# Performance work log

Hardware: AMD Instinct MI355X
Metric: run time of the kernel (lower is better)

## Reference

```python
import jax, jax.numpy as jnp
import numpy as np


def setup_inputs() -> dict:
    key = jax.random.key(0)
    ks = jax.random.split(key, 8)
    B, T, D, E = 16, 1024, 1024, 64
    s = lambda fan: 1.0 / np.sqrt(fan)
    return {
        "seq": jax.random.normal(ks[0], (B, T, D), jnp.float32),
        "pi": jax.random.uniform(ks[1], (E,), jnp.float32),
        "beta_raw": jnp.full((D,), 2.1972246, jnp.float32),  # logit(0.9)
        "p1_w": jax.random.normal(ks[2], (4 * D, 2 * D), jnp.float32) * s(2 * D),
        "p1_b": jnp.zeros((4 * D,), jnp.float32),
        "p2_w": jax.random.normal(ks[3], (D, 4 * D), jnp.float32) * s(4 * D),
        "p2_b": jnp.zeros((D,), jnp.float32),
        "W_w": jax.random.normal(ks[4], (E, D), jnp.float32) * s(D),
        "W_b": jnp.zeros((E,), jnp.float32),
    }


def reference(seq, pi, beta_raw, p1_w, p1_b, p2_w, p2_b, W_w, W_b):
    B, T, D = seq.shape
    beta = jax.nn.sigmoid(beta_raw)  # (D,), per-channel EMA coefficient
    x = jnp.transpose(seq[:, : T - 1, :], (1, 0, 2))  # (T-1, B, D), steps 0..T-2

    # Sequential EMA recurrence h_t = beta*h_{t-1} + x_t (h_{-1}=0)
    def step(h, x_t):
        h = beta * h + x_t
        return h, h

    _, hs = jax.lax.scan(step, jnp.zeros((B, D), seq.dtype), x)  # (T-1, B, D)

    # Predictor MLP over all timesteps at once (use_beta + use_ant branch)
    inp = jnp.concatenate([x, hs], axis=-1)  # (T-1, B, 2D)
    hid = jax.nn.relu(jnp.einsum('tbi,hi->tbh', inp, p1_w) + p1_b)  # (T-1, B, 4D)
    x_hat = jnp.einsum('tbh,dh->tbd', hid, p2_w) + p2_b  # (T-1, B, D)

    # Linear router + pi scaling
    logits = (jnp.einsum('tbd,ed->tbe', x_hat, W_w) + W_b) * pi  # (T-1, B, E)
    return logits, x_hat
```

## Files before the change

kernel.cpp:

```cpp
#include <hip/hip_runtime.h>
#include <hip/hip_bf16.h>
#include <cstdint>
#include <cstddef>

using bf16 = __hip_bfloat16;
typedef __bf16 bf16x8 __attribute__((ext_vector_type(8)));
typedef float f32x4 __attribute__((ext_vector_type(4)));

#define BB 16
#define TT 1024
#define DD 1024
#define EE 64
#define MREAL 16368
#define MPAD  16384
#define NCHUNK 16
#define CHUNK 64

__device__ __forceinline__ void gload_lds16(const void* g, void* l) {
  __builtin_amdgcn_global_load_lds((const __attribute__((address_space(1))) void*)g,
                                   (__attribute__((address_space(3))) void*)l,
                                   16, 0, 0);
}

__device__ __forceinline__ float sigmoidf_(float x) {
  return 1.0f / (1.0f + __expf(-x));
}

__global__ void f2b(const float* __restrict__ src, bf16* __restrict__ dst, int n) {
  int i = (blockIdx.x * blockDim.x + threadIdx.x) * 8;
  if (i < n) {
    float4 v0 = *reinterpret_cast<const float4*>(src + i);
    float4 v1 = *reinterpret_cast<const float4*>(src + i + 4);
    alignas(16) bf16 tmp[8];
    tmp[0] = __float2bfloat16(v0.x); tmp[1] = __float2bfloat16(v0.y);
    tmp[2] = __float2bfloat16(v0.z); tmp[3] = __float2bfloat16(v0.w);
    tmp[4] = __float2bfloat16(v1.x); tmp[5] = __float2bfloat16(v1.y);
    tmp[6] = __float2bfloat16(v1.z); tmp[7] = __float2bfloat16(v1.w);
    *reinterpret_cast<float4*>(dst + i) = *reinterpret_cast<const float4*>(tmp);
  }
}

__global__ void ema_ends(const float* __restrict__ seq, const float* __restrict__ beta_raw,
                         float* __restrict__ ends) {
  int tid = blockIdx.x * blockDim.x + threadIdx.x;
  int d = tid & (DD - 1);
  int b = (tid >> 10) & (BB - 1);
  int c = tid >> 14;
  float beta = sigmoidf_(beta_raw[d]);
  int t0 = c * CHUNK;
  int len = min(CHUNK, (TT - 1) - t0);
  const float* p = seq + (size_t)b * TT * DD + (size_t)t0 * DD + d;
  float h = 0.0f;
#pragma unroll 8
  for (int j = 0; j < len; ++j) h = fmaf(beta, h, p[(size_t)j * DD]);
  ends[tid] = h;
}

__global__ void ema_carry(const float* __restrict__ ends, const float* __restrict__ beta_raw,
                          float* __restrict__ carry) {
  int tid = blockIdx.x * blockDim.x + threadIdx.x;
  int d = tid & (DD - 1);
  float beta = sigmoidf_(beta_raw[d]);
  float bl = beta;
  bl *= bl; bl *= bl; bl *= bl; bl *= bl; bl *= bl; bl *= bl;
  float run = 0.0f;
#pragma unroll
  for (int c = 0; c < NCHUNK; ++c) {
    carry[c * (BB * DD) + tid] = run;
    run = ends[c * (BB * DD) + tid] + bl * run;
  }
}

__global__ void ema_write(const float* __restrict__ seq, const float* __restrict__ beta_raw,
                          const float* __restrict__ carry, bf16* __restrict__ A) {
  int tid = blockIdx.x * blockDim.x + threadIdx.x;
  int d = tid & (DD - 1);
  int b = (tid >> 10) & (BB - 1);
  int c = tid >> 14;
  float beta = sigmoidf_(beta_raw[d]);
  int t0 = c * CHUNK;
  int len = min(CHUNK, (TT - 1) - t0);
  const float* p = seq + (size_t)b * TT * DD + (size_t)t0 * DD + d;
  float h = carry[tid];
#pragma unroll 4
  for (int j = 0; j < len; ++j) {
    float x = p[(size_t)j * DD];
    h = fmaf(beta, h, x);
    size_t m = (size_t)(t0 + j) * BB + b;
    A[m * (2 * DD) + d]      = __float2bfloat16(x);
    A[m * (2 * DD) + DD + d] = __float2bfloat16(h);
  }
}


#define RD_A(d, fb)                                                          \
  _Pragma("unroll")                                                          \
  for (int f = 0; f < 4; ++f)                                                \
    _Pragma("unroll")                                                        \
    for (int s = 0; s < 2; ++s)                                              \
      a[f][s] = *reinterpret_cast<const bf16x8*>(                            \
          &lds[(d) * 32768 + ArdB + ((fb) + f) * 1024 + roff[s]]);

#define RD_B(d, j0)                                                          \
  _Pragma("unroll")                                                          \
  for (int jj = 0; jj < 2; ++jj)                                             \
    _Pragma("unroll")                                                        \
    for (int s = 0; s < 2; ++s)                                              \
      b[(j0) + jj][s] = *reinterpret_cast<const bf16x8*>(                    \
          &lds[(d) * 32768 + BrdB + ((j0) + jj) * 1024 + roff[s]]);

#define STAGE_A(d, h, kq)                                                    \
  {                                                                          \
    _Pragma("unroll")                                                        \
    for (int t = 0; t < 2; ++t)                                              \
      gload_lds16(gA + ((size_t)((h) * 128 + t * 8) * K + (kq) * 64),        \
                  &lds[(d) * 32768 + (h) * 8192 + stbase + t * 512]);        \
  }

#define STAGE_B(d, h, kq)                                                    \
  {                                                                          \
    _Pragma("unroll")                                                        \
    for (int t = 0; t < 2; ++t)                                              \
      gload_lds16(gB + ((size_t)((h) * 128 + t * 8) * K + (kq) * 64),        \
                  &lds[(d) * 32768 + 16384 + (h) * 8192 + stbase + t * 512]); \
  }

#define MFMA_Q(fb, j0)                                                       \
  _Pragma("unroll")                                                          \
  for (int s = 0; s < 2; ++s)                                                \
    _Pragma("unroll")                                                        \
    for (int f = 0; f < 4; ++f)                                              \
      _Pragma("unroll")                                                      \
      for (int j = 0; j < 2; ++j)                                            \
        acc[(fb) + f][(j0) + j] = __builtin_amdgcn_mfma_f32_16x16x32_bf16(   \
            a[f][s], b[(j0) + j][s], acc[(fb) + f][(j0) + j], 0, 0, 0);

#define PH_MID()                                                             \
  __builtin_amdgcn_s_barrier();                                              \
  asm volatile("s_waitcnt lgkmcnt(0)" ::: "memory");                         \
  __builtin_amdgcn_sched_barrier(0);                                         \
  __builtin_amdgcn_s_setprio(1);

#define PH_END()                                                             \
  __builtin_amdgcn_s_setprio(0);                                             \
  __builtin_amdgcn_sched_barrier(0);                                         \
  __builtin_amdgcn_s_barrier();

#define KTILE(d)                                                             \
  {                                                                          \
    const int kA = (q + 1 < NT) ? (q + 1) : (NT - 1);                        \
    const int kB = (q + 2 < NT) ? (q + 2) : (NT - 1);                        \
                                                   \
    RD_A(d, 0);                                                              \
    RD_B(d, 0);                                                              \
    STAGE_A((d) ^ 1, 0, kA);                                                 \
    asm volatile("s_waitcnt lgkmcnt(8)" ::: "memory");                       \
    PH_MID(); MFMA_Q(0, 0); PH_END();                                        \
                                                   \
    RD_B(d, 2);                                                              \
    STAGE_A((d) ^ 1, 1, kA);                                                 \
    PH_MID(); MFMA_Q(0, 2); PH_END();                                        \
                                                   \
    RD_A(d, 4);                                                              \
    STAGE_B((d), 0, kB);                                                     \
    PH_MID(); MFMA_Q(4, 2); PH_END();                                        \
                                                   \
    STAGE_B((d), 1, kB);                                                     \
    asm volatile("s_waitcnt vmcnt(4)" ::: "memory");                         \
    PH_MID(); MFMA_Q(4, 0); PH_END();                                        \
    ++q;                                                                     \
  }

template <bool RELU, bool DUAL_OUT>
__global__ __launch_bounds__(512, 2)
void gemm8(const bf16* __restrict__ A, const bf16* __restrict__ B,
           const float* __restrict__ bias, bf16* __restrict__ outb,
           float* __restrict__ outf, int N, int K) {
  __shared__ bf16 lds[65536];
  const int tid  = threadIdx.x;
  const int wave = tid >> 6;
  const int lane = tid & 63;
  const int wm = wave >> 2;
  const int wn = wave & 3;

  const int gx   = gridDim.x;
  const int nwg  = gx * gridDim.y;
  const int orig = blockIdx.y * gx + blockIdx.x;
  const int swz  = (orig & 7) * (nwg >> 3) + (orig >> 3);
  const int bm = (swz / gx) * 256;
  const int bn = (swz % gx) * 256;

  const int srow = lane >> 3;
  const int scg  = (lane & 7) ^ srow;
  const bf16* gA = A + (size_t)(bm + wave * 16 + srow) * K + scg * 8;
  const bf16* gB = B + (size_t)(bn + wave * 16 + srow) * K + scg * 8;
  const int stbase = wave * 1024;

  int roff[2];
#pragma unroll
  for (int s = 0; s < 2; ++s)
    roff[s] = (lane & 15) * 64 + (((s * 4 + (lane >> 4)) ^ (lane & 7)) * 8);
  const int ArdB = wm * 8192;
  const int BrdB = 16384 + (wn >> 1) * 8192 + (wn & 1) * 4096;

  f32x4 acc[8][4] = {};
  bf16x8 a[4][2], b[4][2];
  const int NT = K >> 6;
  int q = 0;

  STAGE_A(0, 0, 0);
  STAGE_A(0, 1, 0);
  STAGE_B(0, 0, 0);
  STAGE_B(0, 1, 0);
  STAGE_B(1, 0, 1);
  STAGE_B(1, 1, 1);
  asm volatile("s_waitcnt vmcnt(4)" ::: "memory");
  __builtin_amdgcn_s_barrier();

#pragma unroll 1
  for (int it = 0; it < (NT >> 1); ++it) {
    KTILE(0);
    KTILE(1);
  }
  asm volatile("s_waitcnt vmcnt(0)" ::: "memory");

  float bv[4];
  int   ncol[4];
#pragma unroll
  for (int j = 0; j < 4; ++j) {
    ncol[j] = bn + wn * 64 + j * 16 + (lane & 15);
    bv[j]   = bias[ncol[j]];
  }
#pragma unroll
  for (int f = 0; f < 8; ++f) {
    const int m0 = bm + wm * 128 + f * 16 + (lane >> 4) * 4;
#pragma unroll
    for (int j = 0; j < 4; ++j) {
      const int n = ncol[j];
#pragma unroll
      for (int r = 0; r < 4; ++r) {
        float v = acc[f][j][r] + bv[j];
        if (RELU) v = fmaxf(v, 0.0f);
        const int m = m0 + r;
        outb[(size_t)m * N + n] = __float2bfloat16(v);
        if (DUAL_OUT) {
          if (m < MREAL) outf[(size_t)m * N + n] = v;
        }
      }
    }
  }
}

__global__ __launch_bounds__(256)
void gemm_router(const bf16* __restrict__ A, const bf16* __restrict__ B,
                 const float* __restrict__ Wb, const float* __restrict__ pi,
                 float* __restrict__ out) {
  const int K = DD;
  __shared__ alignas(16) bf16 As[64 * 32];
  __shared__ alignas(16) bf16 Bs[64 * 32];
  const int tid  = threadIdx.x;
  const int wave = tid >> 6;
  const int lane = tid & 63;
  const int bm = blockIdx.x * 64;
  const int srow = wave * 16 + (lane >> 2);
  const int scol = (lane & 3) * 8;
  const bf16* gA = A + (size_t)(bm + srow) * K + scol;
  const bf16* gB = B + (size_t)srow * K + scol;
  bf16* lA = &As[srow * 32 + scol];
  bf16* lB = &Bs[srow * 32 + scol];
  const int lr = lane & 15;
  const int quad = lane >> 4;
  f32x4 acc[4] = {};
  for (int k0 = 0; k0 < K; k0 += 32) {
    __syncthreads();
    gload_lds16(gA + k0, lA);
    gload_lds16(gB + k0, lB);
    __syncthreads();
    bf16x8 af = *reinterpret_cast<const bf16x8*>(&As[(wave * 16 + lr) * 32 + quad * 8]);
#pragma unroll
    for (int j = 0; j < 4; ++j) {
      bf16x8 bf_ = *reinterpret_cast<const bf16x8*>(&Bs[(j * 16 + lr) * 32 + quad * 8]);
      acc[j] = __builtin_amdgcn_mfma_f32_16x16x32_bf16(af, bf_, acc[j], 0, 0, 0);
    }
  }
#pragma unroll
  for (int j = 0; j < 4; ++j) {
    const int e = j * 16 + lr;
    const float wb = Wb[e], pv = pi[e];
#pragma unroll
    for (int r = 0; r < 4; ++r) {
      const int m = bm + wave * 16 + quad * 4 + r;
      if (m < MREAL) out[(size_t)m * EE + e] = (acc[j][r] + wb) * pv;
    }
  }
}

extern "C" void kernel_launch(void* const* d_in, const int* in_sizes, int n_in,
                              void* d_out, int out_size, void* d_ws, size_t ws_size,
                              hipStream_t stream) {
  const float* seq      = (const float*)d_in[0];
  const float* pi       = (const float*)d_in[1];
  const float* beta_raw = (const float*)d_in[2];
  const float* p1_w     = (const float*)d_in[3];
  const float* p1_b     = (const float*)d_in[4];
  const float* p2_w     = (const float*)d_in[5];
  const float* p2_b     = (const float*)d_in[6];
  const float* W_w      = (const float*)d_in[7];
  const float* W_b      = (const float*)d_in[8];

  constexpr size_t A_off    = 0;
  constexpr size_t A_sz     = (size_t)MPAD * 2 * DD * sizeof(bf16);
  constexpr size_t W1_off   = A_off + A_sz;
  constexpr size_t W1_sz    = (size_t)4 * DD * 2 * DD * sizeof(bf16);
  constexpr size_t HID_off  = W1_off + W1_sz;
  constexpr size_t HID_sz   = (size_t)MPAD * 4 * DD * sizeof(bf16);
  constexpr size_t W2_off   = HID_off + HID_sz;
  constexpr size_t W2_sz    = (size_t)DD * 4 * DD * sizeof(bf16);
  constexpr size_t W3_off   = W2_off + W2_sz;
  constexpr size_t W3_sz    = (size_t)EE * DD * sizeof(bf16);
  constexpr size_t ENDS_off = W3_off + W3_sz;
  constexpr size_t ENDS_sz  = (size_t)NCHUNK * BB * DD * sizeof(float);
  constexpr size_t CARRY_off = ENDS_off + ENDS_sz;

  char* ws = (char*)d_ws;
  bf16*  Abuf = (bf16*)(ws + A_off);
  bf16*  W1   = (bf16*)(ws + W1_off);
  bf16*  HID  = (bf16*)(ws + HID_off);
  bf16*  W2   = (bf16*)(ws + W2_off);
  bf16*  W3   = (bf16*)(ws + W3_off);
  float* ENDS = (float*)(ws + ENDS_off);
  float* CARRY = (float*)(ws + CARRY_off);
  bf16*  XH   = (bf16*)(ws + A_off);

  float* out_logits = (float*)d_out;
  float* out_xhat   = out_logits + (size_t)MREAL * EE;

  f2b<<<(4 * DD * 2 * DD / 8 + 255) / 256, 256, 0, stream>>>(p1_w, W1, 4 * DD * 2 * DD);
  f2b<<<(DD * 4 * DD / 8 + 255) / 256, 256, 0, stream>>>(p2_w, W2, DD * 4 * DD);
  f2b<<<(EE * DD / 8 + 255) / 256, 256, 0, stream>>>(W_w, W3, EE * DD);

  ema_ends<<<NCHUNK * BB * DD / 256, 256, 0, stream>>>(seq, beta_raw, ENDS);
  ema_carry<<<BB * DD / 256, 256, 0, stream>>>(ENDS, beta_raw, CARRY);
  ema_write<<<NCHUNK * BB * DD / 256, 256, 0, stream>>>(seq, beta_raw, CARRY, Abuf);
  (void)hipMemsetAsync(ws + A_off + (size_t)MREAL * 2 * DD * sizeof(bf16), 0,
                       (size_t)(MPAD - MREAL) * 2 * DD * sizeof(bf16), stream);

  gemm8<true, false><<<dim3(4 * DD / 256, MPAD / 256), 512, 0, stream>>>(
      Abuf, W1, p1_b, HID, nullptr, 4 * DD, 2 * DD);

  gemm8<false, true><<<dim3(DD / 256, MPAD / 256), 512, 0, stream>>>(
      HID, W2, p2_b, XH, out_xhat, DD, 4 * DD);

  gemm_router<<<MPAD / 64, 256, 0, stream>>>(XH, W3, W_b, pi, out_logits);
}
```

Measured before the change: 574.3 us.

## Switch GEMM inner loop to 32x32x16 MFMA with reorganized LDS reads

Replaces the 16x16x32 bf16 MFMA tiling in the main GEMM with 32x32x16 MFMA instructions, each wave holding 4x2 32x32 accumulator tiles. The LDS read pattern, swizzle offsets, phase schedule and epilogue row mapping are rewritten to match the new fragment layout. It also drops the explicit lgkmcnt waits and sched_barriers between phases and leaves wait placement to the compiler. The larger MFMA shape is meant to raise operand reuse per instruction and cut LDS reads and instruction count. The trade-offs are a changed register footprint and possible hazards from the relaxed waits.

```diff
diff --git a/kernel.cpp b/kernel.cpp
--- a/kernel.cpp
+++ b/kernel.cpp
@@ -6,6 +6,7 @@
 using bf16 = __hip_bfloat16;
 typedef __bf16 bf16x8 __attribute__((ext_vector_type(8)));
 typedef float f32x4 __attribute__((ext_vector_type(4)));
+typedef float f32x16 __attribute__((ext_vector_type(16)));
 
 #define BB 16
 #define TT 1024
@@ -93,21 +94,19 @@
 }
 
 
-#define RD_A(d, fb)                                                          \
+#define RD_A2(d, m0)                                                         \
   _Pragma("unroll")                                                          \
-  for (int f = 0; f < 4; ++f)                                                \
+  for (int mf = 0; mf < 2; ++mf)                                             \
     _Pragma("unroll")                                                        \
-    for (int s = 0; s < 2; ++s)                                              \
-      a[f][s] = *reinterpret_cast<const bf16x8*>(                            \
-          &lds[(d) * 32768 + ArdB + ((fb) + f) * 1024 + roff[s]]);
-
-#define RD_B(d, j0)                                                          \
+    for (int ks = 0; ks < 4; ++ks)                                           \
+      a[mf][ks] = *reinterpret_cast<const bf16x8*>(                          \
+          &lds[(d) * 32768 + aB0 + ((m0) + mf) * 2048 + pgs[ks]]);
+
+#define RD_B4(d, nf, breg)                                                   \
   _Pragma("unroll")                                                          \
-  for (int jj = 0; jj < 2; ++jj)                                             \
-    _Pragma("unroll")                                                        \
-    for (int s = 0; s < 2; ++s)                                              \
-      b[(j0) + jj][s] = *reinterpret_cast<const bf16x8*>(                    \
-          &lds[(d) * 32768 + BrdB + ((j0) + jj) * 1024 + roff[s]]);
+  for (int ks = 0; ks < 4; ++ks)                                             \
+    breg[ks] = *reinterpret_cast<const bf16x8*>(                             \
+        &lds[(d) * 32768 + bO[nf] + pgs[ks]]);
 
 #define STAGE_A(d, h, kq)                                                    \
   {                                                                          \
@@ -125,49 +124,42 @@
                   &lds[(d) * 32768 + 16384 + (h) * 8192 + stbase + t * 512]); \
   }
 
-#define MFMA_Q(fb, j0)                                                       \
+#define PH_MFMA(m0, breg, nf)                                                \
+  __builtin_amdgcn_s_barrier();                                              \
+  __builtin_amdgcn_s_setprio(1);                                             \
   _Pragma("unroll")                                                          \
-  for (int s = 0; s < 2; ++s)                                                \
-    _Pragma("unroll")                                                        \
-    for (int f = 0; f < 4; ++f)                                              \
-      _Pragma("unroll")                                                      \
-      for (int j = 0; j < 2; ++j)                                            \
-        acc[(fb) + f][(j0) + j] = __builtin_amdgcn_mfma_f32_16x16x32_bf16(   \
-            a[f][s], b[(j0) + j][s], acc[(fb) + f][(j0) + j], 0, 0, 0);
-
-#define PH_MID()                                                             \
-  __builtin_amdgcn_s_barrier();                                              \
-  asm volatile("s_waitcnt lgkmcnt(0)" ::: "memory");                         \
-  __builtin_amdgcn_sched_barrier(0);                                         \
-  __builtin_amdgcn_s_setprio(1);
-
-#define PH_END()                                                             \
+  for (int ks = 0; ks < 4; ++ks) {                                           \
+    acc[(m0)][nf] = __builtin_amdgcn_mfma_f32_32x32x16_bf16(                 \
+        a[0][ks], breg[ks], acc[(m0)][nf], 0, 0, 0);                         \
+    acc[(m0) + 1][nf] = __builtin_amdgcn_mfma_f32_32x32x16_bf16(             \
+        a[1][ks], breg[ks], acc[(m0) + 1][nf], 0, 0, 0);                     \
+  }                                                                          \
   __builtin_amdgcn_s_setprio(0);                                             \
-  __builtin_amdgcn_sched_barrier(0);                                         \
   __builtin_amdgcn_s_barrier();
 
 #define KTILE(d)                                                             \
   {                                                                          \
     const int kA = (q + 1 < NT) ? (q + 1) : (NT - 1);                        \
     const int kB = (q + 2 < NT) ? (q + 2) : (NT - 1);                        \
-                                                   \
-    RD_A(d, 0);                                                              \
-    RD_B(d, 0);                                                              \
+                                                       \
+    RD_A2(d, 0);                                                             \
+    RD_B4(d, 0, b0);                                                         \
     STAGE_A((d) ^ 1, 0, kA);                                                 \
-    asm volatile("s_waitcnt lgkmcnt(8)" ::: "memory");                       \
-    PH_MID(); MFMA_Q(0, 0); PH_END();                                        \
-                                                   \
-    RD_B(d, 2);                                                              \
+    PH_MFMA(0, b0, 0);                                                       \
+                                                       \
+    RD_B4(d, 1, b1);                                                         \
     STAGE_A((d) ^ 1, 1, kA);                                                 \
-    PH_MID(); MFMA_Q(0, 2); PH_END();                                        \
-                                                   \
-    RD_A(d, 4);                                                              \
+    PH_MFMA(0, b1, 1);                                                       \
+                                                       \
+    RD_A2(d, 2);                                                             \
+    asm volatile("" ::: "memory");   \
     STAGE_B((d), 0, kB);                                                     \
-    PH_MID(); MFMA_Q(4, 2); PH_END();                                        \
-                                                   \
+    PH_MFMA(2, b1, 1);                                                       \
+                                                       \
+    asm volatile("" ::: "memory");                                           \
     STAGE_B((d), 1, kB);                                                     \
     asm volatile("s_waitcnt vmcnt(4)" ::: "memory");                         \
-    PH_MID(); MFMA_Q(4, 0); PH_END();                                        \
+    PH_MFMA(2, b0, 0);                                                       \
     ++q;                                                                     \
   }
 
@@ -196,15 +188,20 @@
   const bf16* gB = B + (size_t)(bn + wave * 16 + srow) * K + scg * 8;
   const int stbase = wave * 1024;
 
-  int roff[2];
-#pragma unroll
-  for (int s = 0; s < 2; ++s)
-    roff[s] = (lane & 15) * 64 + (((s * 4 + (lane >> 4)) ^ (lane & 7)) * 8);
-  const int ArdB = wm * 8192;
-  const int BrdB = 16384 + (wn >> 1) * 8192 + (wn & 1) * 4096;
-
-  f32x4 acc[8][4] = {};
-  bf16x8 a[4][2], b[4][2];
+  int pgs[4];
+#pragma unroll
+  for (int ks = 0; ks < 4; ++ks)
+    pgs[ks] = (((ks * 2 + (lane >> 5)) ^ (lane & 7)) * 8);
+  const int aB0 = wm * 8192 + (lane & 31) * 64;
+  int bO[2];
+#pragma unroll
+  for (int nf = 0; nf < 2; ++nf) {
+    const int rb = wn * 64 + nf * 32 + (lane & 31);
+    bO[nf] = 16384 + (rb >> 7) * 8192 + (rb & 127) * 64;
+  }
+
+  f32x16 acc[4][2] = {};
+  bf16x8 a[2][4], b0[4], b1[4];
   const int NT = K >> 6;
   int q = 0;
 
@@ -224,24 +221,24 @@
   }
   asm volatile("s_waitcnt vmcnt(0)" ::: "memory");
 
-  float bv[4];
-  int   ncol[4];
-#pragma unroll
-  for (int j = 0; j < 4; ++j) {
-    ncol[j] = bn + wn * 64 + j * 16 + (lane & 15);
-    bv[j]   = bias[ncol[j]];
-  }
-#pragma unroll
-  for (int f = 0; f < 8; ++f) {
-    const int m0 = bm + wm * 128 + f * 16 + (lane >> 4) * 4;
-#pragma unroll
-    for (int j = 0; j < 4; ++j) {
-      const int n = ncol[j];
-#pragma unroll
-      for (int r = 0; r < 4; ++r) {
-        float v = acc[f][j][r] + bv[j];
+  float bv[2];
+  int   ncol[2];
+#pragma unroll
+  for (int nf = 0; nf < 2; ++nf) {
+    ncol[nf] = bn + wn * 64 + nf * 32 + (lane & 31);
+    bv[nf]   = bias[ncol[nf]];
+  }
+#pragma unroll
+  for (int mf = 0; mf < 4; ++mf) {
+    const int m0 = bm + wm * 128 + mf * 32 + 4 * (lane >> 5);
+#pragma unroll
+    for (int nf = 0; nf < 2; ++nf) {
+      const int n = ncol[nf];
+#pragma unroll
+      for (int r = 0; r < 16; ++r) {
+        const int m = m0 + (r & 3) + 8 * (r >> 2);
+        float v = acc[mf][nf][r] + bv[nf];
         if (RELU) v = fmaxf(v, 0.0f);
-        const int m = m0 + r;
         outb[(size_t)m * N + n] = __float2bfloat16(v);
         if (DUAL_OUT) {
           if (m < MREAL) outf[(size_t)m * N + n] = v;
```

Result: slower. 606.0 us (+5.5%).

## Software-pipeline LDS fragment reads under MFMA phases in GEMM main loop

Applied to the files above, without the earlier changes.

Restructures the 8-wave GEMM k-loop so that LDS register-fragment reads for the next MFMA quarter are issued in the shadow of the current MFMA block, after the priority drop and before the closing barrier. Register fragments are now double-used across tiles and the B/A read order alternates between the two unrolled k-tiles. This hides LDS read latency behind matrix instructions instead of stalling before each phase. It risks LDS hazards if the barrier and waitcnt placement is wrong, and it raises register pressure.

```diff
diff --git a/kernel.cpp b/kernel.cpp
--- a/kernel.cpp
+++ b/kernel.cpp
@@ -135,41 +135,19 @@
         acc[(fb) + f][(j0) + j] = __builtin_amdgcn_mfma_f32_16x16x32_bf16(   \
             a[f][s], b[(j0) + j][s], acc[(fb) + f][(j0) + j], 0, 0, 0);
 
-#define PH_MID()                                                             \
+#define PH_OPEN()                                                            \
   __builtin_amdgcn_s_barrier();                                              \
   asm volatile("s_waitcnt lgkmcnt(0)" ::: "memory");                         \
   __builtin_amdgcn_sched_barrier(0);                                         \
   __builtin_amdgcn_s_setprio(1);
 
-#define PH_END()                                                             \
+#define PH_SHDW()                                                            \
   __builtin_amdgcn_s_setprio(0);                                             \
+  __builtin_amdgcn_sched_barrier(0);
+
+#define PH_CLOSE()                                                           \
   __builtin_amdgcn_sched_barrier(0);                                         \
   __builtin_amdgcn_s_barrier();
-
-#define KTILE(d)                                                             \
-  {                                                                          \
-    const int kA = (q + 1 < NT) ? (q + 1) : (NT - 1);                        \
-    const int kB = (q + 2 < NT) ? (q + 2) : (NT - 1);                        \
-                                                   \
-    RD_A(d, 0);                                                              \
-    RD_B(d, 0);                                                              \
-    STAGE_A((d) ^ 1, 0, kA);                                                 \
-    asm volatile("s_waitcnt lgkmcnt(8)" ::: "memory");                       \
-    PH_MID(); MFMA_Q(0, 0); PH_END();                                        \
-                                                   \
-    RD_B(d, 2);                                                              \
-    STAGE_A((d) ^ 1, 1, kA);                                                 \
-    PH_MID(); MFMA_Q(0, 2); PH_END();                                        \
-                                                   \
-    RD_A(d, 4);                                                              \
-    STAGE_B((d), 0, kB);                                                     \
-    PH_MID(); MFMA_Q(4, 2); PH_END();                                        \
-                                                   \
-    STAGE_B((d), 1, kB);                                                     \
-    asm volatile("s_waitcnt vmcnt(4)" ::: "memory");                         \
-    PH_MID(); MFMA_Q(4, 0); PH_END();                                        \
-    ++q;                                                                     \
-  }
 
 template <bool RELU, bool DUAL_OUT>
 __global__ __launch_bounds__(512, 2)
@@ -206,7 +184,6 @@
   f32x4 acc[8][4] = {};
   bf16x8 a[4][2], b[4][2];
   const int NT = K >> 6;
-  int q = 0;
 
   STAGE_A(0, 0, 0);
   STAGE_A(0, 1, 0);
@@ -216,11 +193,42 @@
   STAGE_B(1, 1, 1);
   asm volatile("s_waitcnt vmcnt(4)" ::: "memory");
   __builtin_amdgcn_s_barrier();
-
+  RD_A(0, 0);
+  RD_B(0, 0);
+
+  int q = 0;
 #pragma unroll 1
   for (int it = 0; it < (NT >> 1); ++it) {
-    KTILE(0);
-    KTILE(1);
+    {
+      const int kA = (q + 1 < NT) ? (q + 1) : (NT - 1);
+      const int kB = (q + 2 < NT) ? (q + 2) : (NT - 1);
+      STAGE_A(1, 0, kA);
+      PH_OPEN(); MFMA_Q(0, 0); PH_SHDW(); RD_B(0, 2); PH_CLOSE();
+      STAGE_A(1, 1, kA);
+      PH_OPEN(); MFMA_Q(0, 2); PH_SHDW(); RD_A(0, 4); PH_CLOSE();
+      STAGE_B(0, 0, kB);
+      asm volatile("s_waitcnt vmcnt(6)" ::: "memory");
+      PH_OPEN(); MFMA_Q(4, 2); PH_SHDW(); RD_B(1, 2); PH_CLOSE();
+      STAGE_B(0, 1, kB);
+      asm volatile("s_waitcnt vmcnt(4)" ::: "memory");
+      PH_OPEN(); MFMA_Q(4, 0); PH_SHDW(); RD_A(1, 0); PH_CLOSE();
+      ++q;
+    }
+    {
+      const int kA = (q + 1 < NT) ? (q + 1) : (NT - 1);
+      const int kB = (q + 2 < NT) ? (q + 2) : (NT - 1);
+      STAGE_A(0, 0, kA);
+      PH_OPEN(); MFMA_Q(0, 2); PH_SHDW(); RD_B(1, 0); PH_CLOSE();
+      STAGE_A(0, 1, kA);
+      PH_OPEN(); MFMA_Q(0, 0); PH_SHDW(); RD_A(1, 4); PH_CLOSE();
+      STAGE_B(1, 0, kB);
+      asm volatile("s_waitcnt vmcnt(6)" ::: "memory");
+      PH_OPEN(); MFMA_Q(4, 0); PH_SHDW(); RD_B(0, 0); PH_CLOSE();
+      STAGE_B(1, 1, kB);
+      asm volatile("s_waitcnt vmcnt(4)" ::: "memory");
+      PH_OPEN(); MFMA_Q(4, 2); PH_SHDW(); RD_A(0, 0); PH_CLOSE();
+      ++q;
+    }
   }
   asm volatile("s_waitcnt vmcnt(0)" ::: "memory");
 
```

Result: no change. 563.9 us (-1.8%).

## Software-pipeline LDS fragment reads behind MFMA phases with double-buffered registers

Applied to the files above, without the earlier changes.

Restructures the GEMM k-tile loop so that LDS fragment reads for the next phase, and for the next k-tile's A and B tiles from the other LDS buffer, are issued in the shadow of the current phase's MFMAs. Previously each phase read its fragments and then waited on lgkmcnt before computing. B fragments are ping-ponged between two register sets and A is split into halves. Explicit lgkmcnt waits are removed and the vmcnt wait is retimed. The cost is more live VGPRs for the register-resident fragments under a 512x2 launch bound, which risks spills or lower occupancy, and the staging and wait ordering becomes more delicate.

```diff
diff --git a/kernel.cpp b/kernel.cpp
--- a/kernel.cpp
+++ b/kernel.cpp
@@ -93,21 +93,29 @@
 }
 
 
-#define RD_A(d, fb)                                                          \
+#define RD_A03(d)                                                            \
   _Pragma("unroll")                                                          \
   for (int f = 0; f < 4; ++f)                                                \
     _Pragma("unroll")                                                        \
     for (int s = 0; s < 2; ++s)                                              \
-      a[f][s] = *reinterpret_cast<const bf16x8*>(                            \
-          &lds[(d) * 32768 + ArdB + ((fb) + f) * 1024 + roff[s]]);
-
-#define RD_B(d, j0)                                                          \
+      a03[f][s] = *reinterpret_cast<const bf16x8*>(                          \
+          &lds[(d) * 32768 + ArdB + f * 1024 + roff[s]]);
+
+#define RD_A47H(d, f0)                                                       \
+  _Pragma("unroll")                                                          \
+  for (int ff = 0; ff < 2; ++ff)                                             \
+    _Pragma("unroll")                                                        \
+    for (int s = 0; s < 2; ++s)                                              \
+      a47[(f0) + ff][s] = *reinterpret_cast<const bf16x8*>(                  \
+          &lds[(d) * 32768 + ArdB + ((f0) + ff + 4) * 1024 + roff[s]]);
+
+#define RD_B2(d, arr, jbase)                                                 \
   _Pragma("unroll")                                                          \
   for (int jj = 0; jj < 2; ++jj)                                             \
     _Pragma("unroll")                                                        \
     for (int s = 0; s < 2; ++s)                                              \
-      b[(j0) + jj][s] = *reinterpret_cast<const bf16x8*>(                    \
-          &lds[(d) * 32768 + BrdB + ((j0) + jj) * 1024 + roff[s]]);
+      arr[jj][s] = *reinterpret_cast<const bf16x8*>(                         \
+          &lds[(d) * 32768 + BrdB + ((jbase) + jj) * 1024 + roff[s]]);
 
 #define STAGE_A(d, h, kq)                                                    \
   {                                                                          \
@@ -125,7 +133,7 @@
                   &lds[(d) * 32768 + 16384 + (h) * 8192 + stbase + t * 512]); \
   }
 
-#define MFMA_Q(fb, j0)                                                       \
+#define MFMA_P(fb, aarr, j0, barr)                                           \
   _Pragma("unroll")                                                          \
   for (int s = 0; s < 2; ++s)                                                \
     _Pragma("unroll")                                                        \
@@ -133,41 +141,38 @@
       _Pragma("unroll")                                                      \
       for (int j = 0; j < 2; ++j)                                            \
         acc[(fb) + f][(j0) + j] = __builtin_amdgcn_mfma_f32_16x16x32_bf16(   \
-            a[f][s], b[(j0) + j][s], acc[(fb) + f][(j0) + j], 0, 0, 0);
-
-#define PH_MID()                                                             \
+            aarr[f][s], barr[j][s], acc[(fb) + f][(j0) + j], 0, 0, 0);
+
+#define PH_OPEN()                                                            \
   __builtin_amdgcn_s_barrier();                                              \
-  asm volatile("s_waitcnt lgkmcnt(0)" ::: "memory");                         \
-  __builtin_amdgcn_sched_barrier(0);                                         \
   __builtin_amdgcn_s_setprio(1);
 
-#define PH_END()                                                             \
+#define PH_SHDW()                                                            \
   __builtin_amdgcn_s_setprio(0);                                             \
+  __builtin_amdgcn_sched_barrier(0);
+
+#define PH_CLOSE()                                                           \
   __builtin_amdgcn_sched_barrier(0);                                         \
   __builtin_amdgcn_s_barrier();
 
-#define KTILE(d)                                                             \
+#define KTILE2(d, bcur, bnext)                                               \
   {                                                                          \
     const int kA = (q + 1 < NT) ? (q + 1) : (NT - 1);                        \
     const int kB = (q + 2 < NT) ? (q + 2) : (NT - 1);                        \
-                                                   \
-    RD_A(d, 0);                                                              \
-    RD_B(d, 0);                                                              \
+                                                          \
     STAGE_A((d) ^ 1, 0, kA);                                                 \
-    asm volatile("s_waitcnt lgkmcnt(8)" ::: "memory");                       \
-    PH_MID(); MFMA_Q(0, 0); PH_END();                                        \
-                                                   \
-    RD_B(d, 2);                                                              \
+    PH_OPEN(); MFMA_P(0, a03, 0, bcur); PH_SHDW(); RD_A47H(d, 0); PH_CLOSE(); \
+                                                          \
     STAGE_A((d) ^ 1, 1, kA);                                                 \
-    PH_MID(); MFMA_Q(0, 2); PH_END();                                        \
-                                                   \
-    RD_A(d, 4);                                                              \
-    STAGE_B((d), 0, kB);                                                     \
-    PH_MID(); MFMA_Q(4, 2); PH_END();                                        \
-                                                   \
-    STAGE_B((d), 1, kB);                                                     \
-    asm volatile("s_waitcnt vmcnt(4)" ::: "memory");                         \
-    PH_MID(); MFMA_Q(4, 0); PH_END();                                        \
+    PH_OPEN(); MFMA_P(0, a03, 2, b23); PH_SHDW(); RD_A47H(d, 2); PH_CLOSE(); \
+                                                          \
+    STAGE_B(d, 0, kB);                                                       \
+    asm volatile("s_waitcnt vmcnt(2)" ::: "memory");                         \
+    PH_OPEN(); MFMA_P(4, a47, 2, b23); PH_SHDW(); RD_A03((d) ^ 1); PH_CLOSE(); \
+                                                          \
+    STAGE_B(d, 1, kB);                                                       \
+    PH_OPEN(); MFMA_P(4, a47, 0, bcur); PH_SHDW();                           \
+    RD_B2((d) ^ 1, bnext, 0); RD_B2((d) ^ 1, b23, 2); PH_CLOSE();            \
     ++q;                                                                     \
   }
 
@@ -204,9 +209,8 @@
   const int BrdB = 16384 + (wn >> 1) * 8192 + (wn & 1) * 4096;
 
   f32x4 acc[8][4] = {};
-  bf16x8 a[4][2], b[4][2];
+  bf16x8 a03[4][2], a47[4][2], bE[2][2], bO[2][2], b23[2][2];
   const int NT = K >> 6;
-  int q = 0;
 
   STAGE_A(0, 0, 0);
   STAGE_A(0, 1, 0);
@@ -216,11 +220,15 @@
   STAGE_B(1, 1, 1);
   asm volatile("s_waitcnt vmcnt(4)" ::: "memory");
   __builtin_amdgcn_s_barrier();
-
+  RD_A03(0);
+  RD_B2(0, bE, 0);
+  RD_B2(0, b23, 2);
+
+  int q = 0;
 #pragma unroll 1
   for (int it = 0; it < (NT >> 1); ++it) {
-    KTILE(0);
-    KTILE(1);
+    KTILE2(0, bE, bO);
+    KTILE2(1, bO, bE);
   }
   asm volatile("s_waitcnt vmcnt(0)" ::: "memory");
 
```

Result: no change. 579.0 us (+0.8%).
